# Optimization experiments

Hardware: AMD Instinct MI355X
Metric: run time of the kernel (lower is better)

Reference implementation:

```python
import jax, jax.numpy as jnp
import numpy as np

D_MODEL = 1024
N_HEADS = 16
N_KV_HEADS = 4
D_K = D_MODEL // N_HEADS
Q_SIZE = D_MODEL
KV_SIZE = N_KV_HEADS * D_K
QKV_SIZE = Q_SIZE + 2 * KV_SIZE
EPS = 1.1920929e-07  # torch.nn.RMSNorm default eps (fp32 machine eps)
ROPE_BASE = 10000.0


def rms_norm(x, w):
    # normalize over last dim, learned scale (torch nn.RMSNorm)
    return x * jax.lax.rsqrt(jnp.mean(x * x, axis=-1, keepdims=True) + EPS) * w


def rope(x):
    # torchtune RotaryPositionalEmbeddings: interleaved pairs, x is [B,T,H,D]
    T, d = x.shape[1], x.shape[-1]
    inv_freq = 1.0 / (ROPE_BASE ** (jnp.arange(0, d, 2, dtype=jnp.float32) / d))
    ang = jnp.arange(T, dtype=jnp.float32)[:, None] * inv_freq[None, :]  # [T, d/2]
    cos = jnp.cos(ang)[None, :, None, :]
    sin = jnp.sin(ang)[None, :, None, :]
    xr = x.reshape(x.shape[:-1] + (d // 2, 2))
    x1, x2 = xr[..., 0], xr[..., 1]
    out = jnp.stack([x1 * cos - x2 * sin, x1 * sin + x2 * cos], axis=-1)
    return out.reshape(x.shape)


def setup_inputs() -> dict:
    key = jax.random.key(0)
    k1, k2 = jax.random.split(key)
    x = jax.random.normal(k1, (2, 2048, D_MODEL), dtype=jnp.float32)
    qkvo = jax.random.normal(k2, (QKV_SIZE + D_MODEL, D_MODEL), dtype=jnp.float32) * 0.02
    q_norm_w = jnp.ones((D_K,), dtype=jnp.float32)
    k_norm_w = jnp.ones((D_K,), dtype=jnp.float32)
    return {"x": x, "qkvo": qkvo, "q_norm_w": q_norm_w, "k_norm_w": k_norm_w}


def reference(x, qkvo, q_norm_w, k_norm_w):
    B, T, _ = x.shape
    groups = N_HEADS // N_KV_HEADS
    qkv = x @ qkvo[:QKV_SIZE].T  # [B,T,qkv_size]
    Q = qkv[..., :Q_SIZE].reshape(B, T, N_HEADS, D_K)
    K = qkv[..., Q_SIZE:Q_SIZE + KV_SIZE].reshape(B, T, N_KV_HEADS, D_K)
    V = qkv[..., Q_SIZE + KV_SIZE:].reshape(B, T, N_KV_HEADS, D_K)
    Q = rope(rms_norm(Q, q_norm_w))
    K = rope(rms_norm(K, k_norm_w))
    K = jnp.repeat(K, groups, axis=2)  # GQA expand to [B,T,H,D]
    V = jnp.repeat(V, groups, axis=2)
    scale = 1.0 / np.sqrt(D_K).astype(np.float32)
    scores = jnp.einsum('bqhd,bkhd->bhqk', Q, K) * scale
    causal = jnp.tril(jnp.ones((T, T), dtype=bool))
    scores = jnp.where(causal[None, None], scores, jnp.float32(-jnp.inf))
    attn = jax.nn.softmax(scores, axis=-1)
    out = jnp.einsum('bhqk,bkhd->bqhd', attn, V).reshape(B, T, D_MODEL)
    return out @ qkvo[QKV_SIZE:].T
```

## Files before the change

### kernel.cpp

```cpp
#include <hip/hip_runtime.h>
#include <hip/hip_bf16.h>
#include <cstdint>
#include <cstddef>

typedef __bf16 bf16x8 __attribute__((ext_vector_type(8)));
typedef float f32x4 __attribute__((ext_vector_type(4)));

__device__ __forceinline__ unsigned short f2bf(float f) {
    unsigned u = __builtin_bit_cast(unsigned, f);
    u += 0x7FFFu + ((u >> 16) & 1u);
    return (unsigned short)(u >> 16);
}
__device__ __forceinline__ unsigned pk2(float a, float b) {
    typedef __bf16 bf16x2 __attribute__((ext_vector_type(2)));
    bf16x2 h;
    h[0] = (__bf16)a;
    h[1] = (__bf16)b;
    unsigned r;
    __builtin_memcpy(&r, &h, 4);
    return r;
}
__device__ __forceinline__ float fexp2(float x) {
#if __has_builtin(__builtin_amdgcn_exp2f)
    return __builtin_amdgcn_exp2f(x);
#else
    return __expf(x * 0.6931471805599453f);
#endif
}
__device__ __forceinline__ void gld16(const void* g, void* l) {
    __builtin_amdgcn_global_load_lds((const __attribute__((address_space(1))) void*)g,
                                     (__attribute__((address_space(3))) void*)l, 16, 0, 0);
}

__global__ __launch_bounds__(256) void cast_kernel(const float4* __restrict__ x,
                                                   const float4* __restrict__ w,
                                                   ushort4* __restrict__ xbf,
                                                   ushort4* __restrict__ wbf,
                                                   float2* __restrict__ tab) {
    int i = blockIdx.x * 256 + threadIdx.x;
    const int NX4 = 4096 * 1024 / 4;
    const int NW4 = 2560 * 1024 / 4;
    if (i < NX4 + NW4) {
        float4 v;
        ushort4* o;
        if (i < NX4) { v = x[i]; o = xbf + i; }
        else { v = w[i - NX4]; o = wbf + (i - NX4); }
        ushort4 r;
        r.x = f2bf(v.x); r.y = f2bf(v.y); r.z = f2bf(v.z); r.w = f2bf(v.w);
        *o = r;
    } else {
        int k = i - NX4 - NW4;
        if (k >= 2048 * 32) return;
        int t = k >> 5, fp = k & 31;
        float inv = __expf(-(float)(2 * fp) * (1.0f / 64.0f) * 9.210340371976184f);
        float sn, cs;
        sincosf((float)t * inv, &sn, &cs);
        tab[k] = make_float2(cs, sn);
    }
}

__global__ __launch_bounds__(256) void gemm_qkv_fused(const ushort* __restrict__ A,
                                                      const ushort* __restrict__ B,
                                                      const float2* __restrict__ tab,
                                                      const float* __restrict__ qw,
                                                      const float* __restrict__ kw,
                                                      ushort* __restrict__ Qo,
                                                      ushort* __restrict__ Ko,
                                                      ushort* __restrict__ VT) {
    const int K = 1024;
    __shared__ __align__(16) ushort LA[2][4096];
    __shared__ __align__(16) ushort LB[2][8192];
    int tid = threadIdx.x;
    int w = tid >> 6, lane = tid & 63;
    int qm = lane & 15, quad = lane >> 4;

    int nbx = gridDim.x, nby = gridDim.y;
    int nwg = nbx * nby;
    int f = blockIdx.y * nbx + blockIdx.x;
    int q = nwg >> 3, r = nwg & 7;
    int xcd = f & 7, idx = f >> 3;
    int s = (xcd < r ? xcd * (q + 1) : r * (q + 1) + (xcd - r) * q) + idx;
    int m0 = (s / nby) * 64;
    int n0 = (s % nby) * 128;

    int mw = (w & 1) * 32, nw = (w >> 1) * 64;
    int sw = qm & 7;

    f32x4 acc[2][4];
#pragma unroll
    for (int i = 0; i < 2; i++)
#pragma unroll
        for (int j = 0; j < 4; j++) acc[i][j] = (f32x4){0.f, 0.f, 0.f, 0.f};

    int sa[2], ra[2], ga[2];
#pragma unroll
    for (int u = 0; u < 2; u++) {
        sa[u] = tid + u * 256;
        ra[u] = sa[u] >> 3;
        ga[u] = (sa[u] & 7) ^ (ra[u] & 7);
    }
    int sb[4], rb[4], gb[4];
#pragma unroll
    for (int u = 0; u < 4; u++) {
        sb[u] = tid + u * 256;
        rb[u] = sb[u] >> 3;
        gb[u] = (sb[u] & 7) ^ (rb[u] & 7);
    }

    auto do_stage = [&](int k0, int buf) {
#pragma unroll
        for (int u = 0; u < 2; u++)
            gld16(A + (size_t)(m0 + ra[u]) * K + k0 + ga[u] * 8, &LA[buf][sa[u] * 8]);
#pragma unroll
        for (int u = 0; u < 4; u++)
            gld16(B + (size_t)(n0 + rb[u]) * K + k0 + gb[u] * 8, &LB[buf][sb[u] * 8]);
    };

    do_stage(0, 0);
    int buf = 0;
    for (int k0 = 0; k0 < K; k0 += 64, buf ^= 1) {
        __syncthreads();
        if (k0 + 64 < K) do_stage(k0 + 64, buf ^ 1);
        bf16x8 a[2][2], bb[4][2];
#pragma unroll
        for (int mi = 0; mi < 2; mi++)
#pragma unroll
            for (int h = 0; h < 2; h++)
                a[mi][h] = *(const bf16x8*)&LA[buf][((mw + mi * 16 + qm) * 8 + ((h * 4 + quad) ^ sw)) * 8];
#pragma unroll
        for (int ni = 0; ni < 4; ni++)
#pragma unroll
            for (int h = 0; h < 2; h++)
                bb[ni][h] = *(const bf16x8*)&LB[buf][((nw + ni * 16 + qm) * 8 + ((h * 4 + quad) ^ sw)) * 8];
#pragma unroll
        for (int h = 0; h < 2; h++)
#pragma unroll
            for (int mi = 0; mi < 2; mi++)
#pragma unroll
                for (int ni = 0; ni < 4; ni++)
                    acc[mi][ni] = __builtin_amdgcn_mfma_f32_16x16x32_bf16(a[mi][h], bb[ni][h], acc[mi][ni], 0, 0, 0);
    }

    int head_col0 = n0 + nw;
    int rowbase = m0 + mw;
    int b = rowbase >> 11;
    int t0g = rowbase & 2047;
    bool isV = (head_col0 >= 1280);

    __syncthreads();
    if (isV) {
        ushort* lv = &LA[0][0] + w * 2048;
#pragma unroll
        for (int mi = 0; mi < 2; mi++)
#pragma unroll
            for (int r2 = 0; r2 < 4; r2++) {
                int tt = mi * 16 + quad * 4 + r2;
                int pcl = ((tt >> 2) & 3) * 8 + ((tt >> 4) & 1) * 4 + (tt & 3);
#pragma unroll
                for (int ni = 0; ni < 4; ni++)
                    lv[(ni * 16 + qm) * 32 + pcl] = f2bf(acc[mi][ni][r2]);
            }
    } else {
        bool isQ = (head_col0 < 1024);
        const float* wp = isQ ? qw : kw;
        float wt[4];
#pragma unroll
        for (int ni = 0; ni < 4; ni++) wt[ni] = wp[ni * 16 + qm];
        float qs = isQ ? 0.125f : 1.0f;
        ushort* op = isQ ? (Qo + (size_t)(b * 16 + (head_col0 >> 6)) * 2048 * 64)
                         : (Ko + (size_t)(b * 4 + ((head_col0 - 1024) >> 6)) * 2048 * 64);
#pragma unroll
        for (int mi = 0; mi < 2; mi++)
#pragma unroll
            for (int r2 = 0; r2 < 4; r2++) {
                float ssum = acc[mi][0][r2] * acc[mi][0][r2] + acc[mi][1][r2] * acc[mi][1][r2]
                           + acc[mi][2][r2] * acc[mi][2][r2] + acc[mi][3][r2] * acc[mi][3][r2];
                ssum += __shfl_xor(ssum, 1);
                ssum += __shfl_xor(ssum, 2);
                ssum += __shfl_xor(ssum, 4);
                ssum += __shfl_xor(ssum, 8);
                float rinv = rsqrtf(ssum * (1.0f / 64.0f) + 1.1920929e-7f);
                int t = t0g + mi * 16 + quad * 4 + r2;
#pragma unroll
                for (int ni = 0; ni < 4; ni++) {
                    float vn = acc[mi][ni][r2] * rinv * wt[ni];
                    float2 cssn = tab[t * 32 + ni * 8 + (qm >> 1)];
                    float pr = __shfl_xor(vn, 1);
                    float out = (qm & 1) ? fmaf(pr, cssn.y, vn * cssn.x)
                                         : fmaf(vn, cssn.x, -pr * cssn.y);
                    op[(size_t)t * 64 + ni * 16 + qm] = f2bf(out * qs);
                }
            }
    }
    __syncthreads();
    if (isV) {
        const ushort* lv = &LA[0][0] + w * 2048;
        int vh = (head_col0 - 1280) >> 6;
        int bkv = b * 4 + vh;
#pragma unroll
        for (int j = 0; j < 8; j++) {
            int d = j * 8 + (lane >> 3);
            uint2 v = *(const uint2*)&lv[d * 32 + (lane & 7) * 4];
            *(uint2*)&VT[((size_t)(bkv * 64 + d)) * 2048 + t0g + (lane & 7) * 4] = v;
        }
    }
}

__global__ __launch_bounds__(256) void gemm_bf16(const ushort* __restrict__ A,
                                                 const ushort* __restrict__ B,
                                                 float* __restrict__ C,
                                                 int M, int N, int K) {
    __shared__ __align__(16) ushort LA[2][4096];
    __shared__ __align__(16) ushort LB[2][8192];
    int tid = threadIdx.x;
    int w = tid >> 6, lane = tid & 63;
    int qm = lane & 15, quad = lane >> 4;

    int nbx = gridDim.x, nby = gridDim.y;
    int nwg = nbx * nby;
    int f = blockIdx.y * nbx + blockIdx.x;
    int q = nwg >> 3, r = nwg & 7;
    int xcd = f & 7, idx = f >> 3;
    int s = (xcd < r ? xcd * (q + 1) : r * (q + 1) + (xcd - r) * q) + idx;
    int m0 = (s / nby) * 64;
    int n0 = (s % nby) * 128;

    int mw = (w & 1) * 32, nw = (w >> 1) * 64;
    int sw = qm & 7;

    f32x4 acc[2][4];
#pragma unroll
    for (int i = 0; i < 2; i++)
#pragma unroll
        for (int j = 0; j < 4; j++) acc[i][j] = (f32x4){0.f, 0.f, 0.f, 0.f};

    int sa[2], ra[2], ga[2];
#pragma unroll
    for (int u = 0; u < 2; u++) {
        sa[u] = tid + u * 256;
        ra[u] = sa[u] >> 3;
        ga[u] = (sa[u] & 7) ^ (ra[u] & 7);
    }
    int sb[4], rb[4], gb[4];
#pragma unroll
    for (int u = 0; u < 4; u++) {
        sb[u] = tid + u * 256;
        rb[u] = sb[u] >> 3;
        gb[u] = (sb[u] & 7) ^ (rb[u] & 7);
    }

    auto do_stage = [&](int k0, int buf) {
#pragma unroll
        for (int u = 0; u < 2; u++)
            gld16(A + (size_t)(m0 + ra[u]) * K + k0 + ga[u] * 8, &LA[buf][sa[u] * 8]);
#pragma unroll
        for (int u = 0; u < 4; u++)
            gld16(B + (size_t)(n0 + rb[u]) * K + k0 + gb[u] * 8, &LB[buf][sb[u] * 8]);
    };

    do_stage(0, 0);
    int buf = 0;
    for (int k0 = 0; k0 < K; k0 += 64, buf ^= 1) {
        __syncthreads();
        if (k0 + 64 < K) do_stage(k0 + 64, buf ^ 1);
        bf16x8 a[2][2], bb[4][2];
#pragma unroll
        for (int mi = 0; mi < 2; mi++)
#pragma unroll
            for (int h = 0; h < 2; h++)
                a[mi][h] = *(const bf16x8*)&LA[buf][((mw + mi * 16 + qm) * 8 + ((h * 4 + quad) ^ sw)) * 8];
#pragma unroll
        for (int ni = 0; ni < 4; ni++)
#pragma unroll
            for (int h = 0; h < 2; h++)
                bb[ni][h] = *(const bf16x8*)&LB[buf][((nw + ni * 16 + qm) * 8 + ((h * 4 + quad) ^ sw)) * 8];
#pragma unroll
        for (int h = 0; h < 2; h++)
#pragma unroll
            for (int mi = 0; mi < 2; mi++)
#pragma unroll
                for (int ni = 0; ni < 4; ni++)
                    acc[mi][ni] = __builtin_amdgcn_mfma_f32_16x16x32_bf16(a[mi][h], bb[ni][h], acc[mi][ni], 0, 0, 0);
    }
#pragma unroll
    for (int mi = 0; mi < 2; mi++)
#pragma unroll
        for (int ni = 0; ni < 4; ni++) {
            int row = m0 + mw + mi * 16 + quad * 4;
            int col = n0 + nw + ni * 16 + qm;
            float* cp = C + (size_t)row * N + col;
#pragma unroll
            for (int r2 = 0; r2 < 4; r2++) cp[(size_t)r2 * N] = acc[mi][ni][r2];
        }
}

__global__ __launch_bounds__(256) void attn7_kernel(const ushort* __restrict__ Q,
                                                    const ushort* __restrict__ K,
                                                    const ushort* __restrict__ VT,
                                                    ushort* __restrict__ O) {
    __shared__ __align__(16) ushort KT[2][4096];
    __shared__ __align__(16) ushort VL[2][4096];

    const float LOG2E = 1.4426950408889634f;
    const float C8 = 11.541560327111707f;

    int blk = blockIdx.x;
    int qp = 31 - (blk >> 5);
    int bh = blk & 31;
    int tid = threadIdx.x;
    int w = tid >> 6, lane = tid & 63;
    int qm = lane & 15, quad = lane >> 4;
    int b = bh >> 4, h = bh & 15;
    int bkv = b * 4 + (h >> 2);

    const ushort* Qbh = Q + (size_t)bh * 2048 * 64;
    const ushort* Kbh = K + (size_t)bkv * 2048 * 64;
    const ushort* Vbh = VT + (size_t)bkv * 64 * 2048;
    int sw = qm & 7;

    int s0 = tid, s1 = tid + 256;
    int r0 = s0 >> 3, g0 = (s0 & 7) ^ (r0 & 7);
    int r1 = s1 >> 3, g1 = (s1 & 7) ^ (r1 & 7);

    auto do_stage = [&](int j0, int buf) {
        gld16(Kbh + (size_t)(j0 + r0) * 64 + g0 * 8, &KT[buf][s0 * 8]);
        gld16(Kbh + (size_t)(j0 + r1) * 64 + g1 * 8, &KT[buf][s1 * 8]);
        gld16(Vbh + (size_t)r0 * 2048 + j0 + g0 * 8, &VL[buf][s0 * 8]);
        gld16(Vbh + (size_t)r1 * 2048 + j0 + g1 * 8, &VL[buf][s1 * 8]);
    };

    int nch = qp + 1;
    int q0 = qp * 64 + w * 16;
    const ushort* qptr = Qbh + (size_t)(q0 + qm) * 64 + quad * 8;
    bf16x8 qb0 = *(const bf16x8*)qptr;
    bf16x8 qb1 = *(const bf16x8*)(qptr + 32);
    f32x4 oacc[4];
    float lacc = 0.f;
#pragma unroll
    for (int i = 0; i < 4; i++) oacc[i] = (f32x4){0.f, 0.f, 0.f, 0.f};

    do_stage(0, 0);
    int buf = 0;
#pragma unroll 1
    for (int i = 0; i < nch; i++, buf ^= 1) {
        int j0 = i * 64;
        __syncthreads();
        if (i + 1 < nch) do_stage(j0 + 64, buf ^ 1);

        f32x4 st[4];
#pragma unroll
        for (int tj = 0; tj < 4; tj++) st[tj] = (f32x4){0.f, 0.f, 0.f, 0.f};
#pragma unroll
        for (int tj = 0; tj < 4; tj++) {
            bf16x8 kf0 = *(const bf16x8*)&KT[buf][((16 * tj + qm) * 8 + (quad ^ sw)) * 8];
            bf16x8 kf1 = *(const bf16x8*)&KT[buf][((16 * tj + qm) * 8 + ((4 + quad) ^ sw)) * 8];
            st[tj] = __builtin_amdgcn_mfma_f32_16x16x32_bf16(kf0, qb0, st[tj], 0, 0, 0);
            st[tj] = __builtin_amdgcn_mfma_f32_16x16x32_bf16(kf1, qb1, st[tj], 0, 0, 0);
        }
        if (i == nch - 1) {
#pragma unroll
            for (int tj = 0; tj < 4; tj++)
#pragma unroll
                for (int r = 0; r < 4; r++) {
                    int key = j0 + tj * 16 + quad * 4 + r;
                    if (key > q0 + qm) st[tj][r] = -1e30f;
                }
        }
        float rs = 0.f;
#pragma unroll
        for (int tj = 0; tj < 4; tj++)
#pragma unroll
            for (int r = 0; r < 4; r++) {
                float pv = fexp2(fmaf(st[tj][r], LOG2E, -C8));
                st[tj][r] = pv;
                rs += pv;
            }
        lacc += rs;

        unsigned up[4];
        up[0] = pk2(st[0][0], st[0][1]);
        up[1] = pk2(st[0][2], st[0][3]);
        up[2] = pk2(st[1][0], st[1][1]);
        up[3] = pk2(st[1][2], st[1][3]);
        bf16x8 pf0;
        __builtin_memcpy(&pf0, up, 16);
        up[0] = pk2(st[2][0], st[2][1]);
        up[1] = pk2(st[2][2], st[2][3]);
        up[2] = pk2(st[3][0], st[3][1]);
        up[3] = pk2(st[3][2], st[3][3]);
        bf16x8 pf1;
        __builtin_memcpy(&pf1, up, 16);

#pragma unroll
        for (int dt = 0; dt < 4; dt++) {
            bf16x8 vf0 = *(const bf16x8*)&VL[buf][((16 * dt + qm) * 8 + (quad ^ sw)) * 8];
            bf16x8 vf1 = *(const bf16x8*)&VL[buf][((16 * dt + qm) * 8 + ((4 + quad) ^ sw)) * 8];
            oacc[dt] = __builtin_amdgcn_mfma_f32_16x16x32_bf16(vf0, pf0, oacc[dt], 0, 0, 0);
            oacc[dt] = __builtin_amdgcn_mfma_f32_16x16x32_bf16(vf1, pf1, oacc[dt], 0, 0, 0);
        }
    }
    float l = lacc;
    l += __shfl_xor(l, 16);
    l += __shfl_xor(l, 32);
    float rinv = 1.0f / l;
    uint2 val;
#pragma unroll
    for (int dt = 0; dt < 4; dt++) {
        val.x = pk2(oacc[dt][0] * rinv, oacc[dt][1] * rinv);
        val.y = pk2(oacc[dt][2] * rinv, oacc[dt][3] * rinv);
        *(uint2*)&O[((size_t)(b * 2048) + q0 + qm) * 1024 + h * 64 + dt * 16 + quad * 4] = val;
    }
}

extern "C" void kernel_launch(void* const* d_in, const int* in_sizes, int n_in,
                              void* d_out, int out_size, void* d_ws, size_t ws_size,
                              hipStream_t stream) {
    (void)in_sizes; (void)n_in; (void)out_size; (void)ws_size;
    const float* x    = (const float*)d_in[0];
    const float* qkvo = (const float*)d_in[1];
    const float* qw   = (const float*)d_in[2];
    const float* kw   = (const float*)d_in[3];
    float* out = (float*)d_out;

    char* ws = (char*)d_ws;
    ushort* xbf = (ushort*)(ws + 0);
    ushort* wbf = (ushort*)(ws + 8388608);
    float2* tab = (float2*)(ws + 13631488);
    ushort* Qb  = (ushort*)(ws + 38797312);
    ushort* Kb  = (ushort*)(ws + 47185920);
    ushort* VT  = (ushort*)(ws + 49283072);
    ushort* Ob  = (ushort*)(ws + 51380224);

    cast_kernel<<<6912, 256, 0, stream>>>((const float4*)x, (const float4*)qkvo,
                                          (ushort4*)xbf, (ushort4*)wbf, tab);
    gemm_qkv_fused<<<dim3(64, 12), 256, 0, stream>>>(xbf, wbf, tab, qw, kw, Qb, Kb, VT);
    attn7_kernel<<<1024, 256, 0, stream>>>(Qb, Kb, VT, Ob);
    gemm_bf16<<<dim3(64, 8), 256, 0, stream>>>(Ob, wbf + (size_t)1536 * 1024, out, 4096, 1024, 1024);
}
```

Before: 152.5 us.

## Triple-buffer attention K/V tiles with prefetch distance two and regroup heads by KV

The attention kernel moves from double to triple LDS buffering of K and V tiles. It prefetches two chunks ahead and waits with an explicit vmcnt(4) plus s_barrier, so one chunk's loads can stay in flight while the current chunk is computed. It also remaps block indices so that consecutive blocks share the same KV head, which should improve L2 reuse of K/V. LDS use grows from 32KB to 48KB per block, which may lower occupancy.

```diff
diff --git a/kernel.cpp b/kernel.cpp
--- a/kernel.cpp
+++ b/kernel.cpp
@@ -294,24 +294,28 @@
         }
 }
 
-__global__ __launch_bounds__(256) void attn7_kernel(const ushort* __restrict__ Q,
-                                                    const ushort* __restrict__ K,
-                                                    const ushort* __restrict__ VT,
-                                                    ushort* __restrict__ O) {
-    __shared__ __align__(16) ushort KT[2][4096];
-    __shared__ __align__(16) ushort VL[2][4096];
+__global__ __launch_bounds__(256) void attn10_kernel(const ushort* __restrict__ Q,
+                                                     const ushort* __restrict__ K,
+                                                     const ushort* __restrict__ VT,
+                                                     ushort* __restrict__ O) {
+    __shared__ __align__(16) ushort KT[3][4096];
+    __shared__ __align__(16) ushort VL[3][4096];
 
     const float LOG2E = 1.4426950408889634f;
     const float C8 = 11.541560327111707f;
 
     int blk = blockIdx.x;
     int qp = 31 - (blk >> 5);
-    int bh = blk & 31;
+    int low5 = blk & 31;
+    int g = low5 & 7;
+    int hin = low5 >> 3;
+    int b = g >> 2;
+    int h = (g & 3) * 4 + hin;
+    int bh = b * 16 + h;
+    int bkv = g;
     int tid = threadIdx.x;
     int w = tid >> 6, lane = tid & 63;
     int qm = lane & 15, quad = lane >> 4;
-    int b = bh >> 4, h = bh & 15;
-    int bkv = b * 4 + (h >> 2);
 
     const ushort* Qbh = Q + (size_t)bh * 2048 * 64;
     const ushort* Kbh = K + (size_t)bkv * 2048 * 64;
@@ -322,11 +326,11 @@
     int r0 = s0 >> 3, g0 = (s0 & 7) ^ (r0 & 7);
     int r1 = s1 >> 3, g1 = (s1 & 7) ^ (r1 & 7);
 
-    auto do_stage = [&](int j0, int buf) {
-        gld16(Kbh + (size_t)(j0 + r0) * 64 + g0 * 8, &KT[buf][s0 * 8]);
-        gld16(Kbh + (size_t)(j0 + r1) * 64 + g1 * 8, &KT[buf][s1 * 8]);
-        gld16(Vbh + (size_t)r0 * 2048 + j0 + g0 * 8, &VL[buf][s0 * 8]);
-        gld16(Vbh + (size_t)r1 * 2048 + j0 + g1 * 8, &VL[buf][s1 * 8]);
+    auto do_stage = [&](int j0, int bf) {
+        gld16(Kbh + (size_t)(j0 + r0) * 64 + g0 * 8, &KT[bf][s0 * 8]);
+        gld16(Kbh + (size_t)(j0 + r1) * 64 + g1 * 8, &KT[bf][s1 * 8]);
+        gld16(Vbh + (size_t)r0 * 2048 + j0 + g0 * 8, &VL[bf][s0 * 8]);
+        gld16(Vbh + (size_t)r1 * 2048 + j0 + g1 * 8, &VL[bf][s1 * 8]);
     };
 
     int nch = qp + 1;
@@ -340,20 +344,22 @@
     for (int i = 0; i < 4; i++) oacc[i] = (f32x4){0.f, 0.f, 0.f, 0.f};
 
     do_stage(0, 0);
-    int buf = 0;
+    if (nch > 1) do_stage(64, 1);
+    int cur = 0;
 #pragma unroll 1
-    for (int i = 0; i < nch; i++, buf ^= 1) {
+    for (int i = 0; i < nch; i++) {
+        if (i + 1 < nch) asm volatile("s_waitcnt vmcnt(4)\n\ts_barrier" ::: "memory");
+        else             asm volatile("s_waitcnt vmcnt(0)\n\ts_barrier" ::: "memory");
+        if (i + 2 < nch) do_stage((i + 2) * 64, cur == 0 ? 2 : cur - 1);
+
         int j0 = i * 64;
-        __syncthreads();
-        if (i + 1 < nch) do_stage(j0 + 64, buf ^ 1);
-
         f32x4 st[4];
 #pragma unroll
         for (int tj = 0; tj < 4; tj++) st[tj] = (f32x4){0.f, 0.f, 0.f, 0.f};
 #pragma unroll
         for (int tj = 0; tj < 4; tj++) {
-            bf16x8 kf0 = *(const bf16x8*)&KT[buf][((16 * tj + qm) * 8 + (quad ^ sw)) * 8];
-            bf16x8 kf1 = *(const bf16x8*)&KT[buf][((16 * tj + qm) * 8 + ((4 + quad) ^ sw)) * 8];
+            bf16x8 kf0 = *(const bf16x8*)&KT[cur][((16 * tj + qm) * 8 + (quad ^ sw)) * 8];
+            bf16x8 kf1 = *(const bf16x8*)&KT[cur][((16 * tj + qm) * 8 + ((4 + quad) ^ sw)) * 8];
             st[tj] = __builtin_amdgcn_mfma_f32_16x16x32_bf16(kf0, qb0, st[tj], 0, 0, 0);
             st[tj] = __builtin_amdgcn_mfma_f32_16x16x32_bf16(kf1, qb1, st[tj], 0, 0, 0);
         }
@@ -393,11 +399,12 @@
 
 #pragma unroll
         for (int dt = 0; dt < 4; dt++) {
-            bf16x8 vf0 = *(const bf16x8*)&VL[buf][((16 * dt + qm) * 8 + (quad ^ sw)) * 8];
-            bf16x8 vf1 = *(const bf16x8*)&VL[buf][((16 * dt + qm) * 8 + ((4 + quad) ^ sw)) * 8];
+            bf16x8 vf0 = *(const bf16x8*)&VL[cur][((16 * dt + qm) * 8 + (quad ^ sw)) * 8];
+            bf16x8 vf1 = *(const bf16x8*)&VL[cur][((16 * dt + qm) * 8 + ((4 + quad) ^ sw)) * 8];
             oacc[dt] = __builtin_amdgcn_mfma_f32_16x16x32_bf16(vf0, pf0, oacc[dt], 0, 0, 0);
             oacc[dt] = __builtin_amdgcn_mfma_f32_16x16x32_bf16(vf1, pf1, oacc[dt], 0, 0, 0);
         }
+        cur = (cur == 2) ? 0 : cur + 1;
     }
     float l = lacc;
     l += __shfl_xor(l, 16);
@@ -434,6 +441,6 @@
     cast_kernel<<<6912, 256, 0, stream>>>((const float4*)x, (const float4*)qkvo,
                                           (ushort4*)xbf, (ushort4*)wbf, tab);
     gemm_qkv_fused<<<dim3(64, 12), 256, 0, stream>>>(xbf, wbf, tab, qw, kw, Qb, Kb, VT);
-    attn7_kernel<<<1024, 256, 0, stream>>>(Qb, Kb, VT, Ob);
+    attn10_kernel<<<1024, 256, 0, stream>>>(Qb, Kb, VT, Ob);
     gemm_bf16<<<dim3(64, 8), 256, 0, stream>>>(Ob, wbf + (size_t)1536 * 1024, out, 4096, 1024, 1024);
 }
```

Result: no change. 152.5 us (+0.0%).

## Load V fragments directly from global, fold log2e into Q scale, regroup blocks by KV head

Applied to the files above, without the earlier changes.

V tiles are no longer staged through shared memory. Each wave now reads its V MFMA fragments straight from global memory into registers, which halves LDS traffic and capacity. The softmax scale and log2(e) are folded into the Q scale at projection time, so the exp2 argument needs no fma. The constant max-offset subtraction is also dropped, which risks overflow for large scores. Block indices are remapped so that the four query heads sharing a KV head are adjacent, for better L2 reuse of K and V. The cost is uncoalesced, latency-exposed global loads of V inside the inner loop.

```diff
diff --git a/kernel.cpp b/kernel.cpp
--- a/kernel.cpp
+++ b/kernel.cpp
@@ -166,7 +166,7 @@
         float wt[4];
 #pragma unroll
         for (int ni = 0; ni < 4; ni++) wt[ni] = wp[ni * 16 + qm];
-        float qs = isQ ? 0.125f : 1.0f;
+        float qs = isQ ? 0.18033688011112042f : 1.0f;
         ushort* op = isQ ? (Qo + (size_t)(b * 16 + (head_col0 >> 6)) * 2048 * 64)
                          : (Ko + (size_t)(b * 4 + ((head_col0 - 1024) >> 6)) * 2048 * 64);
 #pragma unroll
@@ -294,24 +294,24 @@
         }
 }
 
-__global__ __launch_bounds__(256) void attn7_kernel(const ushort* __restrict__ Q,
-                                                    const ushort* __restrict__ K,
-                                                    const ushort* __restrict__ VT,
-                                                    ushort* __restrict__ O) {
+__global__ __launch_bounds__(256) void attn11_kernel(const ushort* __restrict__ Q,
+                                                     const ushort* __restrict__ K,
+                                                     const ushort* __restrict__ VT,
+                                                     ushort* __restrict__ O) {
     __shared__ __align__(16) ushort KT[2][4096];
-    __shared__ __align__(16) ushort VL[2][4096];
-
-    const float LOG2E = 1.4426950408889634f;
-    const float C8 = 11.541560327111707f;
 
     int blk = blockIdx.x;
     int qp = 31 - (blk >> 5);
-    int bh = blk & 31;
+    int low5 = blk & 31;
+    int g = low5 & 7;
+    int hin = low5 >> 3;
+    int b = g >> 2;
+    int h = (g & 3) * 4 + hin;
+    int bh = b * 16 + h;
+    int bkv = g;
     int tid = threadIdx.x;
     int w = tid >> 6, lane = tid & 63;
     int qm = lane & 15, quad = lane >> 4;
-    int b = bh >> 4, h = bh & 15;
-    int bkv = b * 4 + (h >> 2);
 
     const ushort* Qbh = Q + (size_t)bh * 2048 * 64;
     const ushort* Kbh = K + (size_t)bkv * 2048 * 64;
@@ -322,11 +322,9 @@
     int r0 = s0 >> 3, g0 = (s0 & 7) ^ (r0 & 7);
     int r1 = s1 >> 3, g1 = (s1 & 7) ^ (r1 & 7);
 
-    auto do_stage = [&](int j0, int buf) {
-        gld16(Kbh + (size_t)(j0 + r0) * 64 + g0 * 8, &KT[buf][s0 * 8]);
-        gld16(Kbh + (size_t)(j0 + r1) * 64 + g1 * 8, &KT[buf][s1 * 8]);
-        gld16(Vbh + (size_t)r0 * 2048 + j0 + g0 * 8, &VL[buf][s0 * 8]);
-        gld16(Vbh + (size_t)r1 * 2048 + j0 + g1 * 8, &VL[buf][s1 * 8]);
+    auto do_stage = [&](int j0, int bf) {
+        gld16(Kbh + (size_t)(j0 + r0) * 64 + g0 * 8, &KT[bf][s0 * 8]);
+        gld16(Kbh + (size_t)(j0 + r1) * 64 + g1 * 8, &KT[bf][s1 * 8]);
     };
 
     int nch = qp + 1;
@@ -347,6 +345,15 @@
         __syncthreads();
         if (i + 1 < nch) do_stage(j0 + 64, buf ^ 1);
 
+        bf16x8 vf[4][2];
+        const ushort* vpbase = Vbh + j0 + quad * 8;
+#pragma unroll
+        for (int dt = 0; dt < 4; dt++) {
+            const ushort* vp = vpbase + (size_t)(16 * dt + qm) * 2048;
+            vf[dt][0] = *(const bf16x8*)vp;
+            vf[dt][1] = *(const bf16x8*)(vp + 32);
+        }
+
         f32x4 st[4];
 #pragma unroll
         for (int tj = 0; tj < 4; tj++) st[tj] = (f32x4){0.f, 0.f, 0.f, 0.f};
@@ -371,7 +378,7 @@
         for (int tj = 0; tj < 4; tj++)
 #pragma unroll
             for (int r = 0; r < 4; r++) {
-                float pv = fexp2(fmaf(st[tj][r], LOG2E, -C8));
+                float pv = fexp2(st[tj][r]);
                 st[tj][r] = pv;
                 rs += pv;
             }
@@ -393,10 +400,8 @@
 
 #pragma unroll
         for (int dt = 0; dt < 4; dt++) {
-            bf16x8 vf0 = *(const bf16x8*)&VL[buf][((16 * dt + qm) * 8 + (quad ^ sw)) * 8];
-            bf16x8 vf1 = *(const bf16x8*)&VL[buf][((16 * dt + qm) * 8 + ((4 + quad) ^ sw)) * 8];
-            oacc[dt] = __builtin_amdgcn_mfma_f32_16x16x32_bf16(vf0, pf0, oacc[dt], 0, 0, 0);
-            oacc[dt] = __builtin_amdgcn_mfma_f32_16x16x32_bf16(vf1, pf1, oacc[dt], 0, 0, 0);
+            oacc[dt] = __builtin_amdgcn_mfma_f32_16x16x32_bf16(vf[dt][0], pf0, oacc[dt], 0, 0, 0);
+            oacc[dt] = __builtin_amdgcn_mfma_f32_16x16x32_bf16(vf[dt][1], pf1, oacc[dt], 0, 0, 0);
         }
     }
     float l = lacc;
@@ -434,6 +439,6 @@
     cast_kernel<<<6912, 256, 0, stream>>>((const float4*)x, (const float4*)qkvo,
                                           (ushort4*)xbf, (ushort4*)wbf, tab);
     gemm_qkv_fused<<<dim3(64, 12), 256, 0, stream>>>(xbf, wbf, tab, qw, kw, Qb, Kb, VT);
-    attn7_kernel<<<1024, 256, 0, stream>>>(Qb, Kb, VT, Ob);
+    attn11_kernel<<<1024, 256, 0, stream>>>(Qb, Kb, VT, Ob);
     gemm_bf16<<<dim3(64, 8), 256, 0, stream>>>(Ob, wbf + (size_t)1536 * 1024, out, 4096, 1024, 1024);
 }
```

Result: slower. 194.3 us (+27.4%).
